# Kernel tuning notes

Hardware: AMD Instinct MI355X
Metric: run time of the kernel (lower is better)

The kernel has to match this reference:

```python
import jax, jax.numpy as jnp
import numpy as np

N = 8192
EPS = 1e-6


def setup_inputs() -> dict:
    key = jax.random.key(0)
    k1, k2, k3, k4 = jax.random.split(key, 4)
    P_risk = jax.random.normal(k1, (N,), dtype=jnp.float32)
    P_surv = jax.random.normal(k2, (N,), dtype=jnp.float32)
    T = jax.random.uniform(k3, (N,), dtype=jnp.float32)
    E = jax.random.randint(k4, (N,), 0, 2, dtype=jnp.int32)
    return {"P_risk": P_risk, "P_surv": P_surv, "T": T, "E": E}


def _compute_loss(P, M, E_eff):
    # P: [N] log-hazards, M: [N, N] float mask, E_eff: [N] effective event weights
    P_exp = jnp.exp(P)
    # sum_j M[i, j] * exp(P[j])  -- masked risk-set sum as a matvec
    P_exp_sum = M @ P_exp
    log_ratio = jnp.log(P_exp / (P_exp_sum + EPS))
    return -jnp.sum(log_ratio * E_eff) / jnp.sum(E_eff)


def reference(P_risk, P_surv, T, E):
    Ef = E.astype(jnp.float32)
    # M_risk[i, j] = 1 if T[i] < T[j]
    M_risk = (T[:, None] < T[None, :]).astype(jnp.float32)
    # M_surv[i, j] = 1 if T[i] > T[j] and E[j] == 1
    M_surv = (T[:, None] > T[None, :]).astype(jnp.float32) * Ef[None, :]

    # mode='risk': E * (row of M_risk nonempty)
    E_risk = Ef * (jnp.sum(M_risk, axis=1) > 0).astype(jnp.float32)
    # mode='surv': just (row of M_surv nonempty)
    E_surv = (jnp.sum(M_surv, axis=1) > 0).astype(jnp.float32)

    loss_risk = _compute_loss(P_risk, M_risk, E_risk)
    loss_surv = _compute_loss(P_surv, M_surv, E_surv)
    return (loss_risk, loss_surv)
```

## Files before the change

kernel.cpp:

```cpp
#include <hip/hip_runtime.h>
#include <math.h>

#define NN 8192
#define EPSF 1e-6f
#define R 8
#define GX (NN / R)


__global__ __launch_bounds__(256) void ds_prep(
    const float* __restrict__ Pr, const float* __restrict__ Ps,
    const float* __restrict__ T,  const int* __restrict__ E,
    float4* __restrict__ pack) {
  int i = blockIdx.x * 256 + threadIdx.x;
  float t  = T[i];
  float er = __expf(Pr[i]);
  float es = E[i] ? __expf(Ps[i]) : 0.0f;
  pack[i] = make_float4(t, er, es, 0.0f);
}

__global__ __launch_bounds__(256) void ds_main(
    const float* __restrict__ T, const float4* __restrict__ pack,
    float* __restrict__ sumR, float* __restrict__ sumS) {
  const int row0 = blockIdx.x * R;
  const int tid  = threadIdx.x;

  float Ti[R];
#pragma unroll
  for (int r = 0; r < R; ++r) Ti[r] = T[row0 + r];

  float sr[R], ss[R];
#pragma unroll
  for (int r = 0; r < R; ++r) { sr[r] = 0.0f; ss[r] = 0.0f; }

  for (int k = 0; k < NN; k += 256 * 4) {
    float4 p0 = pack[k + tid];
    float4 p1 = pack[k + 256 + tid];
    float4 p2 = pack[k + 512 + tid];
    float4 p3 = pack[k + 768 + tid];
#pragma unroll
    for (int r = 0; r < R; ++r) {
      bool g0 = p0.x > Ti[r];
      sr[r] += g0 ? p0.y : 0.0f;  ss[r] += g0 ? 0.0f : p0.z;
      bool g1 = p1.x > Ti[r];
      sr[r] += g1 ? p1.y : 0.0f;  ss[r] += g1 ? 0.0f : p1.z;
      bool g2 = p2.x > Ti[r];
      sr[r] += g2 ? p2.y : 0.0f;  ss[r] += g2 ? 0.0f : p2.z;
      bool g3 = p3.x > Ti[r];
      sr[r] += g3 ? p3.y : 0.0f;  ss[r] += g3 ? 0.0f : p3.z;
    }
  }

#pragma unroll
  for (int r = 0; r < R; ++r) {
    for (int off = 32; off > 0; off >>= 1) {
      sr[r] += __shfl_down(sr[r], off);
      ss[r] += __shfl_down(ss[r], off);
    }
  }
  __shared__ float sh[4][2 * R];
  const int wid = tid >> 6, lane = tid & 63;
  if (lane == 0) {
#pragma unroll
    for (int r = 0; r < R; ++r) { sh[wid][r] = sr[r]; sh[wid][R + r] = ss[r]; }
  }
  __syncthreads();
  if (tid < 2 * R) {
    float v = sh[0][tid] + sh[1][tid] + sh[2][tid] + sh[3][tid];
    if (tid < R) {
      sumR[row0 + tid] = v;
    } else {
      int r = tid - R;
      sumS[row0 + r] = v - pack[row0 + r].z;
    }
  }
}

__global__ __launch_bounds__(1024) void ds_finalize(
    const float* __restrict__ Pr, const float* __restrict__ Ps,
    const int* __restrict__ E,
    const float* __restrict__ sumR, const float* __restrict__ sumS,
    float* __restrict__ out) {
  float nr = 0.0f, dr = 0.0f, ns = 0.0f, ds = 0.0f;
  for (int i = threadIdx.x; i < NN; i += 1024) {
    float srv = sumR[i];
    float ssv = sumS[i];
    float er = (E[i] != 0 && srv > 0.0f) ? 1.0f : 0.0f;
    float es = (ssv > 0.0f) ? 1.0f : 0.0f;
    nr += er * (Pr[i] - logf(srv + EPSF));
    dr += er;
    ns += es * (Ps[i] - logf(ssv + EPSF));
    ds += es;
  }
  for (int off = 32; off > 0; off >>= 1) {
    nr += __shfl_down(nr, off);
    dr += __shfl_down(dr, off);
    ns += __shfl_down(ns, off);
    ds += __shfl_down(ds, off);
  }
  __shared__ float sh[4][16];
  int wid  = threadIdx.x >> 6;
  int lane = threadIdx.x & 63;
  if (lane == 0) {
    sh[0][wid] = nr; sh[1][wid] = dr; sh[2][wid] = ns; sh[3][wid] = ds;
  }
  __syncthreads();
  if (threadIdx.x == 0) {
    float NR = 0, DR = 0, NS = 0, DS = 0;
#pragma unroll
    for (int w = 0; w < 16; ++w) {
      NR += sh[0][w]; DR += sh[1][w]; NS += sh[2][w]; DS += sh[3][w];
    }
    out[0] = -NR / DR;
    out[1] = -NS / DS;
  }
}

extern "C" void kernel_launch(void* const* d_in, const int* in_sizes, int n_in,
                              void* d_out, int out_size, void* d_ws, size_t ws_size,
                              hipStream_t stream) {
  const float* Pr = (const float*)d_in[0];
  const float* Ps = (const float*)d_in[1];
  const float* T  = (const float*)d_in[2];
  const int*   E  = (const int*)d_in[3];
  float* out = (float*)d_out;

  char* ws = (char*)d_ws;
  float4* pack = (float4*)ws;
  float*  sumR = (float*)(ws + (size_t)NN * sizeof(float4));
  float*  sumS = sumR + NN;

  ds_prep<<<NN / 256, 256, 0, stream>>>(Pr, Ps, T, E, pack);
  ds_main<<<GX, 256, 0, stream>>>(T, pack, sumR, sumS);
  ds_finalize<<<1, 1024, 0, stream>>>(Pr, Ps, E, sumR, sumS, out);
}
```

Measured before the change: 76.70 us.

## Fuse finalize into main kernel via last-block ticket and double rows per block

```diff
diff --git a/kernel.cpp b/kernel.cpp
--- a/kernel.cpp
+++ b/kernel.cpp
@@ -3,26 +3,33 @@
 
 #define NN 8192
 #define EPSF 1e-6f
-#define R 8
+#define R 16
 #define GX (NN / R)
 
 
 __global__ __launch_bounds__(256) void ds_prep(
     const float* __restrict__ Pr, const float* __restrict__ Ps,
     const float* __restrict__ T,  const int* __restrict__ E,
-    float4* __restrict__ pack) {
+    float4* __restrict__ pack, float* __restrict__ sumR, float* __restrict__ sumS,
+    unsigned int* __restrict__ ticket) {
   int i = blockIdx.x * 256 + threadIdx.x;
   float t  = T[i];
   float er = __expf(Pr[i]);
   float es = E[i] ? __expf(Ps[i]) : 0.0f;
   pack[i] = make_float4(t, er, es, 0.0f);
+  sumR[i] = 0.0f;
+  sumS[i] = 0.0f;
+  if (i == 0) *ticket = 0u;
 }
 
 __global__ __launch_bounds__(256) void ds_main(
     const float* __restrict__ T, const float4* __restrict__ pack,
-    float* __restrict__ sumR, float* __restrict__ sumS) {
+    const float* __restrict__ Pr, const float* __restrict__ Ps,
+    const int* __restrict__ E,
+    float* __restrict__ sumR, float* __restrict__ sumS,
+    unsigned int* __restrict__ ticket, float* __restrict__ out) {
+  const int tid  = threadIdx.x;
   const int row0 = blockIdx.x * R;
-  const int tid  = threadIdx.x;
 
   float Ti[R];
 #pragma unroll
@@ -67,49 +74,47 @@
   if (tid < 2 * R) {
     float v = sh[0][tid] + sh[1][tid] + sh[2][tid] + sh[3][tid];
     if (tid < R) {
-      sumR[row0 + tid] = v;
+      atomicAdd(&sumR[row0 + tid], v);
     } else {
       int r = tid - R;
-      sumS[row0 + r] = v - pack[row0 + r].z;
+      atomicAdd(&sumS[row0 + r], v - pack[row0 + r].z);
     }
   }
-}
+  __threadfence();
+  __syncthreads();
 
-__global__ __launch_bounds__(1024) void ds_finalize(
-    const float* __restrict__ Pr, const float* __restrict__ Ps,
-    const int* __restrict__ E,
-    const float* __restrict__ sumR, const float* __restrict__ sumS,
-    float* __restrict__ out) {
-  float nr = 0.0f, dr = 0.0f, ns = 0.0f, ds = 0.0f;
-  for (int i = threadIdx.x; i < NN; i += 1024) {
-    float srv = sumR[i];
-    float ssv = sumS[i];
+  __shared__ unsigned int my_ticket;
+  if (tid == 0) my_ticket = atomicAdd(ticket, 1u);
+  __syncthreads();
+  if (my_ticket != (unsigned int)(GX - 1)) return;
+
+  float nr = 0.0f, dr = 0.0f, ns = 0.0f, nds = 0.0f;
+  for (int i = tid; i < NN; i += 256) {
+    float srv = atomicAdd(&sumR[i], 0.0f);
+    float ssv = atomicAdd(&sumS[i], 0.0f);
     float er = (E[i] != 0 && srv > 0.0f) ? 1.0f : 0.0f;
     float es = (ssv > 0.0f) ? 1.0f : 0.0f;
-    nr += er * (Pr[i] - logf(srv + EPSF));
-    dr += er;
-    ns += es * (Ps[i] - logf(ssv + EPSF));
-    ds += es;
+    nr  += er * (Pr[i] - logf(srv + EPSF));
+    dr  += er;
+    ns  += es * (Ps[i] - logf(ssv + EPSF));
+    nds += es;
   }
   for (int off = 32; off > 0; off >>= 1) {
-    nr += __shfl_down(nr, off);
-    dr += __shfl_down(dr, off);
-    ns += __shfl_down(ns, off);
-    ds += __shfl_down(ds, off);
+    nr  += __shfl_down(nr,  off);
+    dr  += __shfl_down(dr,  off);
+    ns  += __shfl_down(ns,  off);
+    nds += __shfl_down(nds, off);
   }
-  __shared__ float sh[4][16];
-  int wid  = threadIdx.x >> 6;
-  int lane = threadIdx.x & 63;
+  __shared__ float fin[4][4];
   if (lane == 0) {
-    sh[0][wid] = nr; sh[1][wid] = dr; sh[2][wid] = ns; sh[3][wid] = ds;
+    fin[0][wid] = nr; fin[1][wid] = dr; fin[2][wid] = ns; fin[3][wid] = nds;
   }
   __syncthreads();
-  if (threadIdx.x == 0) {
-    float NR = 0, DR = 0, NS = 0, DS = 0;
-#pragma unroll
-    for (int w = 0; w < 16; ++w) {
-      NR += sh[0][w]; DR += sh[1][w]; NS += sh[2][w]; DS += sh[3][w];
-    }
+  if (tid == 0) {
+    float NR = fin[0][0] + fin[0][1] + fin[0][2] + fin[0][3];
+    float DR = fin[1][0] + fin[1][1] + fin[1][2] + fin[1][3];
+    float NS = fin[2][0] + fin[2][1] + fin[2][2] + fin[2][3];
+    float DS = fin[3][0] + fin[3][1] + fin[3][2] + fin[3][3];
     out[0] = -NR / DR;
     out[1] = -NS / DS;
   }
@@ -128,8 +133,8 @@
   float4* pack = (float4*)ws;
   float*  sumR = (float*)(ws + (size_t)NN * sizeof(float4));
   float*  sumS = sumR + NN;
+  unsigned int* ticket = (unsigned int*)(sumS + NN);
 
-  ds_prep<<<NN / 256, 256, 0, stream>>>(Pr, Ps, T, E, pack);
-  ds_main<<<GX, 256, 0, stream>>>(T, pack, sumR, sumS);
-  ds_finalize<<<1, 1024, 0, stream>>>(Pr, Ps, E, sumR, sumS, out);
+  ds_prep<<<NN / 256, 256, 0, stream>>>(Pr, Ps, T, E, pack, sumR, sumS, ticket);
+  ds_main<<<GX, 256, 0, stream>>>(T, pack, Pr, Ps, E, sumR, sumS, ticket, out);
 }
```

New measurement: 115.0 us. +50.0%, slower.
